# Performance work log

Hardware: AMD Instinct MI355X
Metric: run time of the kernel (lower is better)

The kernel has to match this reference:

```python
import jax, jax.numpy as jnp
import numpy as np

N_HEAD = 4
D_HEAD = 16
LN_EPS = 1e-5


def setup_inputs() -> dict:
    key = jax.random.key(0)
    ks = jax.random.split(key, 16)
    B, T, N, F = 4, 64, 325, 3
    d, D = D_HEAD, N_HEAD * D_HEAD
    inputs = jax.random.normal(ks[0], (B, T, N, F), dtype=jnp.float32)
    # row-scaled random adjacency keeps Chebyshev polynomials well-conditioned
    adj = jax.random.uniform(ks[1], (N, N), dtype=jnp.float32) / N
    s = 0.05
    w_lt = jax.random.normal(ks[2], (d, F), dtype=jnp.float32) * s   # Conv2d(F,d,1x1) weight
    b_lt = jnp.zeros((d,), jnp.float32)
    wq = jax.random.normal(ks[3], (d, D), dtype=jnp.float32) * s
    bq = jnp.zeros((D,), jnp.float32)
    wk = jax.random.normal(ks[4], (d, D), dtype=jnp.float32) * s
    bk = jnp.zeros((D,), jnp.float32)
    wv = jax.random.normal(ks[5], (d, D), dtype=jnp.float32) * s
    bv = jnp.zeros((D,), jnp.float32)
    w_ls = jax.random.normal(ks[6], (d, D), dtype=jnp.float32) * s   # Conv2d(D,d,1x1) weight
    b_ls = jnp.zeros((d,), jnp.float32)
    gamma = jnp.ones((d, T, N), jnp.float32)
    beta = jnp.zeros((d, T, N), jnp.float32)
    return dict(inputs=inputs, adj=adj, w_lt=w_lt, b_lt=b_lt, wq=wq, bq=bq,
                wk=wk, bk=bk, wv=wv, bv=bv, w_ls=w_ls, b_ls=b_ls,
                gamma=gamma, beta=beta)


def _graphcn(x, adj, w, b):
    # x: (B,T,N,d); Chebyshev supports k=3; einsum 'kij,jbtf->bitf' sums over k,
    # so it is equivalent to one matmul with the summed support.
    N = adj.shape[0]
    I = jnp.eye(N, dtype=adj.dtype)
    S = I + adj + (2.0 * adj @ adj - I)          # sum of T0, T1, T2
    lfs = jnp.einsum('ij,btjf->btif', S, x)      # (B,T,N,d)
    return jax.nn.relu(lfs @ w + b)              # (B,T,N,D)


def reference(inputs, adj, w_lt, b_lt, wq, bq, wk, bk, wv, bv, w_ls, b_ls, gamma, beta):
    B, T, N, F = inputs.shape
    h, d = N_HEAD, D_HEAD
    # LinearTrans 1x1 conv: (B,T,N,F) -> (B,d,T,N)
    X = jax.nn.relu(jnp.einsum('btnf,of->botn', inputs, w_lt) + b_lt[None, :, None, None])
    rescon = X
    Xp = jnp.transpose(X, (0, 2, 3, 1))          # (B,T,N,d)
    Q = _graphcn(Xp, adj, wq, bq)                # (B,T,N,D)
    K = _graphcn(Xp, adj, wk, bk)
    V = _graphcn(Xp, adj, wv, bv)

    def split_heads(A):
        # torch split(dim=1 channels)+cat(dim=0) == heads leading: (h,B,N,T,d)
        return jnp.transpose(A.reshape(B, T, N, h, d), (3, 0, 2, 1, 4))

    Qh, Kh, Vh = split_heads(Q), split_heads(K), split_heads(V)
    scores = jnp.einsum('hbntd,hbnsd->hbnts', Qh, Kh) / (d ** 0.5)  # (h,B,N,T,T)
    attn = jax.nn.softmax(scores, axis=-1)
    mask = jnp.tril(jnp.ones((T, T), bool))      # mask applied AFTER softmax, as in source
    attn = jnp.where(mask, attn, jnp.asarray(1e-9, attn.dtype))
    res = jax.nn.relu(jnp.einsum('hbnts,hbnsd->hbntd', attn, Vh))   # (h,B,N,T,d)
    # split(dim=0 by batch)+cat(dim=-1): heads back to channel dim
    res = jnp.transpose(res, (1, 2, 3, 0, 4)).reshape(B, N, T, h * d)  # (B,N,T,D)
    res = jnp.transpose(res, (0, 3, 2, 1))       # (B,D,T,N)
    res = jax.nn.relu(jnp.einsum('od,bdtn->botn', w_ls, res) + b_ls[None, :, None, None])  # (B,d,T,N)
    y = rescon + res
    mu = jnp.mean(y, axis=(1, 2, 3), keepdims=True)
    var = jnp.var(y, axis=(1, 2, 3), keepdims=True)
    y = (y - mu) * jax.lax.rsqrt(var + LN_EPS) * gamma[None] + beta[None]
    return jnp.transpose(y, (0, 2, 3, 1))        # (B,T,N,d)
```

## Files before the change

### kernel.cpp

```cpp
#include <hip/hip_runtime.h>
#include <hip/hip_bf16.h>

#define B_ 4
#define T_ 64
#define N_ 325
#define NP 336
#define F_ 3
#define DH 16
#define DD 64
#define NH 4
#define BT_ 256
#define M_ 4096

using f16x4 = __attribute__((ext_vector_type(4))) _Float16;
using f32x4 = __attribute__((ext_vector_type(4))) float;
#define MFMA16 __builtin_amdgcn_mfma_f32_16x16x16f16

__global__ __launch_bounds__(256) void k_prep(const float* __restrict__ adj,
                                              const float* __restrict__ in,
                                              const float* __restrict__ w,
                                              const float* __restrict__ bias,
                                              _Float16* __restrict__ S16,
                                              _Float16* __restrict__ X16) {
    int tid = threadIdx.x;
    if (blockIdx.x < 126) {
        __shared__ __align__(16) float red[4][16][68];
        int sb = blockIdx.x;
        int j0 = (sb % 6) * 64;
        int i0 = (sb / 6) * 16;
        int w4 = tid >> 6, l = tid & 63;
        int lr = l & 15, kg = l >> 4;
        int c0 = w4 * 5;
        int nc = (w4 == 3) ? 6 : 5;

        f32x4 acc0 = {0.f,0.f,0.f,0.f}, acc1 = acc0, acc2 = acc0, acc3 = acc0;
        int I = i0 + lr;
        for (int cc = 0; cc < nc; ++cc) {
            int kb = (c0 + cc) * 16 + kg * 4;
            f16x4 af, b0, b1, b2, b3;
#pragma unroll
            for (int j = 0; j < 4; ++j) {
                int k = kb + j;
                af[j] = (I < N_ && k < N_) ? (_Float16)adj[I * N_ + k] : (_Float16)0.f;
                _Float16 x0 = (_Float16)0.f, x1 = x0, x2 = x0, x3 = x0;
                if (k < N_) {
                    const float* ar = adj + (size_t)k * N_;
                    int m0 = j0 + lr;
                    if (m0 < N_)      x0 = (_Float16)ar[m0];
                    if (m0 + 16 < N_) x1 = (_Float16)ar[m0 + 16];
                    if (m0 + 32 < N_) x2 = (_Float16)ar[m0 + 32];
                    if (m0 + 48 < N_) x3 = (_Float16)ar[m0 + 48];
                }
                b0[j] = x0; b1[j] = x1; b2[j] = x2; b3[j] = x3;
            }
            acc0 = MFMA16(af, b0, acc0, 0, 0, 0);
            acc1 = MFMA16(af, b1, acc1, 0, 0, 0);
            acc2 = MFMA16(af, b2, acc2, 0, 0, 0);
            acc3 = MFMA16(af, b3, acc3, 0, 0, 0);
        }
#pragma unroll
        for (int r = 0; r < 4; ++r) {
            red[w4][kg * 4 + r][ 0 + lr] = acc0[r];
            red[w4][kg * 4 + r][16 + lr] = acc1[r];
            red[w4][kg * 4 + r][32 + lr] = acc2[r];
            red[w4][kg * 4 + r][48 + lr] = acc3[r];
        }
        __syncthreads();
        int row = tid >> 4, col = (tid & 15) * 4;
        int I2 = i0 + row;
#pragma unroll
        for (int q = 0; q < 4; ++q) {
            int J = j0 + col + q;
            if (J < NP) {
                float v = 0.f;
                if (I2 < N_ && J < N_) {
                    float r4 = ((red[0][row][col + q] + red[1][row][col + q]) +
                                (red[2][row][col + q] + red[3][row][col + q]));
                    v = adj[I2 * N_ + J] + 2.f * r4;
                }
                S16[I2 * NP + J] = (_Float16)v;
            }
        }
    } else {
        int idx4 = ((blockIdx.x - 126) * 256 + tid) * 4;
        if (idx4 >= N_ * M_) return;
        int n = idx4 >> 12;
        int r = idx4 & 4095;
        int bt = r >> 4, c0 = r & 15;
        int tok = bt * N_ + n;
        float f0 = in[tok * 3 + 0];
        float f1 = in[tok * 3 + 1];
        float f2 = in[tok * 3 + 2];
        f16x4 o;
        o[0] = (_Float16)fmaxf(bias[c0+0] + f0*w[(c0+0)*3+0] + f1*w[(c0+0)*3+1] + f2*w[(c0+0)*3+2], 0.f);
        o[1] = (_Float16)fmaxf(bias[c0+1] + f0*w[(c0+1)*3+0] + f1*w[(c0+1)*3+1] + f2*w[(c0+1)*3+2], 0.f);
        o[2] = (_Float16)fmaxf(bias[c0+2] + f0*w[(c0+2)*3+0] + f1*w[(c0+2)*3+1] + f2*w[(c0+2)*3+2], 0.f);
        o[3] = (_Float16)fmaxf(bias[c0+3] + f0*w[(c0+3)*3+0] + f1*w[(c0+3)*3+1] + f2*w[(c0+3)*3+2], 0.f);
        *(f16x4*)&X16[idx4] = o;
    }
}

__global__ __launch_bounds__(256) void k_gconv(const _Float16* __restrict__ S16,
                                               const _Float16* __restrict__ X16,
                                               _Float16* __restrict__ lfs16) {
    __shared__ __align__(16) float red[4][16][68];
    int m0 = blockIdx.x * 64;
    int i0 = blockIdx.y * 16;
    int tid = threadIdx.x;
    int w = tid >> 6, l = tid & 63;
    int lr = l & 15, kg = l >> 4;

    int c0 = w * 5;
    int nc = (w == 3) ? 6 : 5;

    f32x4 acc0 = {0.f,0.f,0.f,0.f}, acc1 = acc0, acc2 = acc0, acc3 = acc0;
    const size_t arow = (size_t)(i0 + lr) * NP;
    for (int cc = 0; cc < nc; ++cc) {
        int kb = (c0 + cc) * 16 + kg * 4;
        f16x4 af = *(const f16x4*)&S16[arow + kb];
        f16x4 b0, b1, b2, b3;
#pragma unroll
        for (int j = 0; j < 4; ++j) {
            int k = kb + j;
            _Float16 x0 = (_Float16)0.f, x1 = x0, x2 = x0, x3 = x0;
            if (k < N_) {
                const _Float16* xr = X16 + (size_t)k * M_ + m0;
                x0 = xr[lr]; x1 = xr[16 + lr]; x2 = xr[32 + lr]; x3 = xr[48 + lr];
            }
            b0[j] = x0; b1[j] = x1; b2[j] = x2; b3[j] = x3;
        }
        acc0 = MFMA16(af, b0, acc0, 0, 0, 0);
        acc1 = MFMA16(af, b1, acc1, 0, 0, 0);
        acc2 = MFMA16(af, b2, acc2, 0, 0, 0);
        acc3 = MFMA16(af, b3, acc3, 0, 0, 0);
    }
#pragma unroll
    for (int r = 0; r < 4; ++r) {
        red[w][kg * 4 + r][ 0 + lr] = acc0[r];
        red[w][kg * 4 + r][16 + lr] = acc1[r];
        red[w][kg * 4 + r][32 + lr] = acc2[r];
        red[w][kg * 4 + r][48 + lr] = acc3[r];
    }
    __syncthreads();
    int row = tid >> 4, col = (tid & 15) * 4;
    if (i0 + row < N_) {
        float4 p0 = *(const float4*)&red[0][row][col];
        float4 p1 = *(const float4*)&red[1][row][col];
        float4 p2 = *(const float4*)&red[2][row][col];
        float4 p3 = *(const float4*)&red[3][row][col];
        f16x4 o;
        o[0] = (_Float16)((p0.x + p1.x) + (p2.x + p3.x));
        o[1] = (_Float16)((p0.y + p1.y) + (p2.y + p3.y));
        o[2] = (_Float16)((p0.z + p1.z) + (p2.z + p3.z));
        o[3] = (_Float16)((p0.w + p1.w) + (p2.w + p3.w));
        *(f16x4*)&lfs16[(size_t)(i0 + row) * M_ + m0 + col] = o;
    }
}

__global__ __launch_bounds__(256) void k_attn(
    const _Float16* __restrict__ lfs16, const float* __restrict__ in,
    const float* __restrict__ wlt, const float* __restrict__ blt,
    const float* __restrict__ wq, const float* __restrict__ bq,
    const float* __restrict__ wk, const float* __restrict__ bk,
    const float* __restrict__ wv, const float* __restrict__ bv,
    const float* __restrict__ wls, const float* __restrict__ bls,
    _Float16* __restrict__ ypre16, float* __restrict__ part) {
    __shared__ __align__(16) float Rs[NH][T_][20];
    __shared__ float lnp[NH][2];
    int bn = blockIdx.x;
    int b = bn / N_, n = bn % N_;
    int tid = threadIdx.x;
    int h = tid >> 6;
    int l = tid & 63;
    int lr = l & 15, kg = l >> 4;

    const _Float16* Lsrc = lfs16 + (size_t)n * M_ + b * (T_ * DH);
    f16x4 lff[4];
#pragma unroll
    for (int q = 0; q < 4; ++q)
        lff[q] = *(const f16x4*)&Lsrc[(lr + 16 * q) * DH + kg * 4];

    f16x4 wqf, wkf, wvf, wlf;
    {
        int base = h * 16 + lr;
#pragma unroll
        for (int j = 0; j < 4; ++j) {
            wqf[j] = (_Float16)wq[(kg * 4 + j) * DD + base];
            wkf[j] = (_Float16)wk[(kg * 4 + j) * DD + base];
            wvf[j] = (_Float16)wv[(kg * 4 + j) * DD + base];
        }
        const float4 w4 = *(const float4*)&wls[lr * DD + h * 16 + kg * 4];
        wlf[0] = (_Float16)w4.x; wlf[1] = (_Float16)w4.y; wlf[2] = (_Float16)w4.z; wlf[3] = (_Float16)w4.w;
    }
    f32x4 zero = {0.f, 0.f, 0.f, 0.f};

    f16x4 qtf[4], ktf[4], vvf[4];
    {
        float bqr[4], bkr[4];
#pragma unroll
        for (int r = 0; r < 4; ++r) { bqr[r] = bq[h * 16 + kg * 4 + r]; bkr[r] = bk[h * 16 + kg * 4 + r]; }
        float bvc = bv[h * 16 + lr];
#pragma unroll
        for (int q = 0; q < 4; ++q) {
            f32x4 qa = MFMA16(wqf, lff[q], zero, 0, 0, 0);
            f32x4 ka = MFMA16(wkf, lff[q], zero, 0, 0, 0);
            f32x4 va = MFMA16(lff[q], wvf, zero, 0, 0, 0);
#pragma unroll
            for (int r = 0; r < 4; ++r) {
                qtf[q][r] = (_Float16)(fmaxf(qa[r] + bqr[r], 0.f) * 0.25f);
                ktf[q][r] = (_Float16)fmaxf(ka[r] + bkr[r], 0.f);
                vvf[q][r] = (_Float16)fmaxf(va[r] + bvc, 0.f);
            }
        }
    }

#pragma unroll
    for (int tt = 0; tt < 4; ++tt) {
        f32x4 stc[4];
#pragma unroll
        for (int ss = 0; ss < 4; ++ss)
            stc[ss] = MFMA16(ktf[ss], qtf[tt], zero, 0, 0, 0);
        int t = tt * 16 + lr;
        float m = -1e30f;
#pragma unroll
        for (int ss = 0; ss < 4; ++ss)
#pragma unroll
            for (int r = 0; r < 4; ++r) m = fmaxf(m, stc[ss][r]);
        m = fmaxf(m, __shfl_xor(m, 16));
        m = fmaxf(m, __shfl_xor(m, 32));
        float e[4][4];
        float sum = 0.f;
#pragma unroll
        for (int ss = 0; ss < 4; ++ss)
#pragma unroll
            for (int r = 0; r < 4; ++r) { float ev = __expf(stc[ss][r] - m); e[ss][r] = ev; sum += ev; }
        sum += __shfl_xor(sum, 16);
        sum += __shfl_xor(sum, 32);
        float inv = 1.f / sum;
        f16x4 pc[4];
#pragma unroll
        for (int ss = 0; ss < 4; ++ss)
#pragma unroll
            for (int r = 0; r < 4; ++r) {
                int s = ss * 16 + kg * 4 + r;
                pc[ss][r] = (s <= t) ? (_Float16)(e[ss][r] * inv) : (_Float16)0.f;
            }
        f32x4 acc = zero;
#pragma unroll
        for (int ss = 0; ss < 4; ++ss)
            acc = MFMA16(vvf[ss], pc[ss], acc, 0, 0, 0);
        f16x4 rt;
#pragma unroll
        for (int r = 0; r < 4; ++r) rt[r] = (_Float16)fmaxf(acc[r], 0.f);
        f32x4 rp = MFMA16(wlf, rt, zero, 0, 0, 0);
        float4 o4; o4.x = rp[0]; o4.y = rp[1]; o4.z = rp[2]; o4.w = rp[3];
        *(float4*)&Rs[h][t][kg * 4] = o4;
    }
    __syncthreads();

    {
        int t = tid >> 2, o0 = (tid & 3) * 4;
        float4 r0 = *(const float4*)&Rs[0][t][o0];
        float4 r1 = *(const float4*)&Rs[1][t][o0];
        float4 r2 = *(const float4*)&Rs[2][t][o0];
        float4 r3 = *(const float4*)&Rs[3][t][o0];
        int tok = ((b * T_ + t) * N_ + n) * 3;
        float f0 = in[tok], f1 = in[tok + 1], f2 = in[tok + 2];
        float xv[4];
#pragma unroll
        for (int i = 0; i < 4; ++i) {
            int c = o0 + i;
            xv[i] = fmaxf(blt[c] + f0 * wlt[c * 3 + 0] + f1 * wlt[c * 3 + 1] + f2 * wlt[c * 3 + 2], 0.f);
        }
        float y0 = xv[0] + fmaxf(r0.x + r1.x + r2.x + r3.x + bls[o0 + 0], 0.f);
        float y1 = xv[1] + fmaxf(r0.y + r1.y + r2.y + r3.y + bls[o0 + 1], 0.f);
        float y2 = xv[2] + fmaxf(r0.z + r1.z + r2.z + r3.z + bls[o0 + 2], 0.f);
        float y3 = xv[3] + fmaxf(r0.w + r1.w + r2.w + r3.w + bls[o0 + 3], 0.f);
        f16x4 yv16;
        yv16[0] = (_Float16)y0; yv16[1] = (_Float16)y1;
        yv16[2] = (_Float16)y2; yv16[3] = (_Float16)y3;
        *(f16x4*)&ypre16[(size_t)b * 332800 + (size_t)n * 1024 + t * DH + o0] = yv16;
        float ls = (y0 + y1) + (y2 + y3);
        float lq = (y0 * y0 + y1 * y1) + (y2 * y2 + y3 * y3);
#pragma unroll
        for (int off = 32; off > 0; off >>= 1) { ls += __shfl_down(ls, off); lq += __shfl_down(lq, off); }
        if (l == 0) { lnp[h][0] = ls; lnp[h][1] = lq; }
    }
    __syncthreads();
    if (tid == 0) {
        part[bn * 2]     = (lnp[0][0] + lnp[1][0]) + (lnp[2][0] + lnp[3][0]);
        part[bn * 2 + 1] = (lnp[0][1] + lnp[1][1]) + (lnp[2][1] + lnp[3][1]);
    }
}

__global__ __launch_bounds__(256) void k_lnapply(const _Float16* __restrict__ y16,
                                                 const float* __restrict__ part,
                                                 const float* __restrict__ gamma,
                                                 const float* __restrict__ beta,
                                                 float* __restrict__ out) {
    __shared__ float gs[N_ * DH];
    __shared__ float bs[N_ * DH];
    __shared__ float ssum[256], ssq[256];
    int blk = blockIdx.x, tid = threadIdx.x;
    int b = blk >> 6, t = blk & 63;
    for (int i = tid; i < N_ * DH; i += 256) {
        int c = i / N_, n = i - c * N_;
        size_t g = (size_t)(c * T_ + t) * N_ + n;
        gs[i] = gamma[g];
        bs[i] = beta[g];
    }
    float s = 0.f, q = 0.f;
    for (int i = tid; i < N_; i += 256) {
        s += part[(b * N_ + i) * 2];
        q += part[(b * N_ + i) * 2 + 1];
    }
    ssum[tid] = s; ssq[tid] = q;
    __syncthreads();
    for (int st = 128; st > 0; st >>= 1) {
        if (tid < st) { ssum[tid] += ssum[tid + st]; ssq[tid] += ssq[tid + st]; }
        __syncthreads();
    }
    float mu = ssum[0] / 332800.f;
    float rs = rsqrtf(ssq[0] / 332800.f - mu * mu + 1e-5f);

    float* ob = out + (size_t)(b * T_ + t) * (N_ * DH);
    const _Float16* yb = y16 + (size_t)b * 332800 + t * DH;
    for (int e = tid; e < N_ * DH; e += 256) {
        int n = e >> 4, c = e & 15;
        float yv = (float)yb[(size_t)n * 1024 + c];
        ob[e] = (yv - mu) * rs * gs[c * N_ + n] + bs[c * N_ + n];
    }
}

extern "C" void kernel_launch(void* const* d_in, const int* in_sizes, int n_in,
                              void* d_out, int out_size, void* d_ws, size_t ws_size,
                              hipStream_t stream) {
    const float* in   = (const float*)d_in[0];
    const float* adj  = (const float*)d_in[1];
    const float* w_lt = (const float*)d_in[2];
    const float* b_lt = (const float*)d_in[3];
    const float* wq   = (const float*)d_in[4];
    const float* bq   = (const float*)d_in[5];
    const float* wk   = (const float*)d_in[6];
    const float* bk   = (const float*)d_in[7];
    const float* wv   = (const float*)d_in[8];
    const float* bv   = (const float*)d_in[9];
    const float* wls  = (const float*)d_in[10];
    const float* bls  = (const float*)d_in[11];
    const float* gam  = (const float*)d_in[12];
    const float* bet  = (const float*)d_in[13];
    float* out = (float*)d_out;

    float* ws = (float*)d_ws;
    _Float16* S16 = (_Float16*)ws;
    _Float16* X16 = (_Float16*)(ws + 56576);
    _Float16* lfs16 = (_Float16*)(ws + 56576 + 665600);
    _Float16* ypre16 = (_Float16*)(ws + 56576 + 665600 + 665600);
    float* part = ws + 56576 + 665600 + 665600 + 665600;

    k_prep<<<126 + 1300, 256, 0, stream>>>(adj, in, w_lt, b_lt, S16, X16);
    k_gconv<<<dim3(64, 21), 256, 0, stream>>>(S16, X16, lfs16);
    k_attn<<<B_ * N_, 256, 0, stream>>>(lfs16, in, w_lt, b_lt, wq, bq, wk, bk, wv, bv, wls, bls, ypre16, part);
    k_lnapply<<<B_ * T_, 256, 0, stream>>>(ypre16, part, gam, bet, out);
}
```

Baseline: 61.12 us.

## Transpose X to K-contiguous layout and give each wave its own gconv tile

```diff
diff --git a/kernel.cpp b/kernel.cpp
--- a/kernel.cpp
+++ b/kernel.cpp
@@ -18,10 +18,10 @@
 
 __global__ __launch_bounds__(256) void k_prep(const float* __restrict__ adj,
                                               const float* __restrict__ in,
-                                              const float* __restrict__ w,
-                                              const float* __restrict__ bias,
+                                              const float* __restrict__ wlt,
+                                              const float* __restrict__ blt,
                                               _Float16* __restrict__ S16,
-                                              _Float16* __restrict__ X16) {
+                                              _Float16* __restrict__ X16T) {
     int tid = threadIdx.x;
     if (blockIdx.x < 126) {
         __shared__ __align__(16) float red[4][16][68];
@@ -32,7 +32,6 @@
         int lr = l & 15, kg = l >> 4;
         int c0 = w4 * 5;
         int nc = (w4 == 3) ? 6 : 5;
-
         f32x4 acc0 = {0.f,0.f,0.f,0.f}, acc1 = acc0, acc2 = acc0, acc3 = acc0;
         int I = i0 + lr;
         for (int cc = 0; cc < nc; ++cc) {
@@ -82,78 +81,56 @@
             }
         }
     } else {
-        int idx4 = ((blockIdx.x - 126) * 256 + tid) * 4;
-        if (idx4 >= N_ * M_) return;
-        int n = idx4 >> 12;
-        int r = idx4 & 4095;
-        int bt = r >> 4, c0 = r & 15;
-        int tok = bt * N_ + n;
-        float f0 = in[tok * 3 + 0];
-        float f1 = in[tok * 3 + 1];
-        float f2 = in[tok * 3 + 2];
+        int idx = (blockIdx.x - 126) * 256 + tid;
+        int m = idx / 84;
+        int n0 = (idx - m * 84) * 4;
+        int bt = m >> 4, c = m & 15;
+        float w0 = wlt[c * 3 + 0], w1 = wlt[c * 3 + 1], w2 = wlt[c * 3 + 2];
+        float bb = blt[c];
         f16x4 o;
-        o[0] = (_Float16)fmaxf(bias[c0+0] + f0*w[(c0+0)*3+0] + f1*w[(c0+0)*3+1] + f2*w[(c0+0)*3+2], 0.f);
-        o[1] = (_Float16)fmaxf(bias[c0+1] + f0*w[(c0+1)*3+0] + f1*w[(c0+1)*3+1] + f2*w[(c0+1)*3+2], 0.f);
-        o[2] = (_Float16)fmaxf(bias[c0+2] + f0*w[(c0+2)*3+0] + f1*w[(c0+2)*3+1] + f2*w[(c0+2)*3+2], 0.f);
-        o[3] = (_Float16)fmaxf(bias[c0+3] + f0*w[(c0+3)*3+0] + f1*w[(c0+3)*3+1] + f2*w[(c0+3)*3+2], 0.f);
-        *(f16x4*)&X16[idx4] = o;
+#pragma unroll
+        for (int j = 0; j < 4; ++j) {
+            int n = n0 + j;
+            float v = 0.f;
+            if (n < N_) {
+                const float* ip = in + ((size_t)bt * N_ + n) * 3;
+                v = fmaxf(bb + ip[0] * w0 + ip[1] * w1 + ip[2] * w2, 0.f);
+            }
+            o[j] = (_Float16)v;
+        }
+        *(f16x4*)&X16T[(size_t)m * NP + n0] = o;
     }
 }
 
 __global__ __launch_bounds__(256) void k_gconv(const _Float16* __restrict__ S16,
-                                               const _Float16* __restrict__ X16,
+                                               const _Float16* __restrict__ X16T,
                                                _Float16* __restrict__ lfs16) {
-    __shared__ __align__(16) float red[4][16][68];
-    int m0 = blockIdx.x * 64;
-    int i0 = blockIdx.y * 16;
     int tid = threadIdx.x;
     int w = tid >> 6, l = tid & 63;
     int lr = l & 15, kg = l >> 4;
-
-    int c0 = w * 5;
-    int nc = (w == 3) ? 6 : 5;
-
-    f32x4 acc0 = {0.f,0.f,0.f,0.f}, acc1 = acc0, acc2 = acc0, acc3 = acc0;
-    const size_t arow = (size_t)(i0 + lr) * NP;
-    for (int cc = 0; cc < nc; ++cc) {
-        int kb = (c0 + cc) * 16 + kg * 4;
-        f16x4 af = *(const f16x4*)&S16[arow + kb];
-        f16x4 b0, b1, b2, b3;
-#pragma unroll
-        for (int j = 0; j < 4; ++j) {
-            int k = kb + j;
-            _Float16 x0 = (_Float16)0.f, x1 = x0, x2 = x0, x3 = x0;
-            if (k < N_) {
-                const _Float16* xr = X16 + (size_t)k * M_ + m0;
-                x0 = xr[lr]; x1 = xr[16 + lr]; x2 = xr[32 + lr]; x3 = xr[48 + lr];
-            }
-            b0[j] = x0; b1[j] = x1; b2[j] = x2; b3[j] = x3;
-        }
+    int vt = blockIdx.x * 4 + w;
+    int m0 = (vt & 127) * 32;
+    int i0 = (vt >> 7) * 16;
+    f32x4 acc0 = {0.f,0.f,0.f,0.f}, acc1 = acc0;
+    const _Float16* Arow = S16 + (size_t)(i0 + lr) * NP;
+    const _Float16* Br0 = X16T + (size_t)(m0 + lr) * NP;
+    const _Float16* Br1 = X16T + (size_t)(m0 + 16 + lr) * NP;
+#pragma unroll 3
+    for (int c = 0; c < 21; ++c) {
+        int kb = c * 16 + kg * 4;
+        f16x4 af = *(const f16x4*)&Arow[kb];
+        f16x4 b0 = *(const f16x4*)&Br0[kb];
+        f16x4 b1 = *(const f16x4*)&Br1[kb];
         acc0 = MFMA16(af, b0, acc0, 0, 0, 0);
         acc1 = MFMA16(af, b1, acc1, 0, 0, 0);
-        acc2 = MFMA16(af, b2, acc2, 0, 0, 0);
-        acc3 = MFMA16(af, b3, acc3, 0, 0, 0);
     }
 #pragma unroll
     for (int r = 0; r < 4; ++r) {
-        red[w][kg * 4 + r][ 0 + lr] = acc0[r];
-        red[w][kg * 4 + r][16 + lr] = acc1[r];
-        red[w][kg * 4 + r][32 + lr] = acc2[r];
-        red[w][kg * 4 + r][48 + lr] = acc3[r];
-    }
-    __syncthreads();
-    int row = tid >> 4, col = (tid & 15) * 4;
-    if (i0 + row < N_) {
-        float4 p0 = *(const float4*)&red[0][row][col];
-        float4 p1 = *(const float4*)&red[1][row][col];
-        float4 p2 = *(const float4*)&red[2][row][col];
-        float4 p3 = *(const float4*)&red[3][row][col];
-        f16x4 o;
-        o[0] = (_Float16)((p0.x + p1.x) + (p2.x + p3.x));
-        o[1] = (_Float16)((p0.y + p1.y) + (p2.y + p3.y));
-        o[2] = (_Float16)((p0.z + p1.z) + (p2.z + p3.z));
-        o[3] = (_Float16)((p0.w + p1.w) + (p2.w + p3.w));
-        *(f16x4*)&lfs16[(size_t)(i0 + row) * M_ + m0 + col] = o;
+        int row = i0 + kg * 4 + r;
+        if (row < N_) {
+            lfs16[(size_t)row * M_ + m0 + lr]      = (_Float16)acc0[r];
+            lfs16[(size_t)row * M_ + m0 + 16 + lr] = (_Float16)acc1[r];
+        }
     }
 }
 
@@ -293,30 +270,30 @@
     }
 }
 
-__global__ __launch_bounds__(256) void k_lnapply(const _Float16* __restrict__ y16,
-                                                 const float* __restrict__ part,
-                                                 const float* __restrict__ gamma,
-                                                 const float* __restrict__ beta,
-                                                 float* __restrict__ out) {
+__global__ __launch_bounds__(1024) void k_lnapply(const _Float16* __restrict__ y16,
+                                                  const float* __restrict__ part,
+                                                  const float* __restrict__ gamma,
+                                                  const float* __restrict__ beta,
+                                                  float* __restrict__ out) {
     __shared__ float gs[N_ * DH];
-    __shared__ float bs[N_ * DH];
-    __shared__ float ssum[256], ssq[256];
+    __shared__ float bsh[N_ * DH];
+    __shared__ float ssum[1024], ssq[1024];
     int blk = blockIdx.x, tid = threadIdx.x;
     int b = blk >> 6, t = blk & 63;
-    for (int i = tid; i < N_ * DH; i += 256) {
+    for (int i = tid; i < N_ * DH; i += 1024) {
         int c = i / N_, n = i - c * N_;
         size_t g = (size_t)(c * T_ + t) * N_ + n;
         gs[i] = gamma[g];
-        bs[i] = beta[g];
+        bsh[i] = beta[g];
     }
     float s = 0.f, q = 0.f;
-    for (int i = tid; i < N_; i += 256) {
-        s += part[(b * N_ + i) * 2];
-        q += part[(b * N_ + i) * 2 + 1];
+    if (tid < N_) {
+        s = part[(b * N_ + tid) * 2];
+        q = part[(b * N_ + tid) * 2 + 1];
     }
     ssum[tid] = s; ssq[tid] = q;
     __syncthreads();
-    for (int st = 128; st > 0; st >>= 1) {
+    for (int st = 512; st > 0; st >>= 1) {
         if (tid < st) { ssum[tid] += ssum[tid + st]; ssq[tid] += ssq[tid + st]; }
         __syncthreads();
     }
@@ -325,10 +302,10 @@
 
     float* ob = out + (size_t)(b * T_ + t) * (N_ * DH);
     const _Float16* yb = y16 + (size_t)b * 332800 + t * DH;
-    for (int e = tid; e < N_ * DH; e += 256) {
+    for (int e = tid; e < N_ * DH; e += 1024) {
         int n = e >> 4, c = e & 15;
         float yv = (float)yb[(size_t)n * 1024 + c];
-        ob[e] = (yv - mu) * rs * gs[c * N_ + n] + bs[c * N_ + n];
+        ob[e] = (yv - mu) * rs * gs[c * N_ + n] + bsh[c * N_ + n];
     }
 }
 
@@ -352,14 +329,14 @@
     float* out = (float*)d_out;
 
     float* ws = (float*)d_ws;
-    _Float16* S16 = (_Float16*)ws;
-    _Float16* X16 = (_Float16*)(ws + 56576);
-    _Float16* lfs16 = (_Float16*)(ws + 56576 + 665600);
-    _Float16* ypre16 = (_Float16*)(ws + 56576 + 665600 + 665600);
-    float* part = ws + 56576 + 665600 + 665600 + 665600;
-
-    k_prep<<<126 + 1300, 256, 0, stream>>>(adj, in, w_lt, b_lt, S16, X16);
-    k_gconv<<<dim3(64, 21), 256, 0, stream>>>(S16, X16, lfs16);
+    _Float16* S16   = (_Float16*)ws;
+    _Float16* X16T  = (_Float16*)(ws + 56576);
+    _Float16* lfs16 = (_Float16*)(ws + 56576 + 688128);
+    _Float16* ypre16= (_Float16*)(ws + 56576 + 688128 + 665600);
+    float* part = ws + 56576 + 688128 + 665600 + 665600;
+
+    k_prep<<<126 + 1344, 256, 0, stream>>>(adj, in, w_lt, b_lt, S16, X16T);
+    k_gconv<<<672, 256, 0, stream>>>(S16, X16T, lfs16);
     k_attn<<<B_ * N_, 256, 0, stream>>>(lfs16, in, w_lt, b_lt, wq, bq, wk, bk, wv, bv, wls, bls, ypre16, part);
-    k_lnapply<<<B_ * T_, 256, 0, stream>>>(ypre16, part, gam, bet, out);
-}
+    k_lnapply<<<B_ * T_, 1024, 0, stream>>>(ypre16, part, gam, bet, out);
+}
```

Measured after the change: 64.95 us. 1.06x slower.
